# Optimization experiments

Hardware: AMD Instinct MI355X
Metric: run time of the kernel (lower is better)

Reference implementation:

```python
import jax, jax.numpy as jnp
import numpy as np

N_NODES = 100000
N_EDGES = 3200000
N_RELS = 8
F_IN = 64
F_OUT = 64


def setup_inputs() -> dict:
    key = jax.random.key(0)
    k1, k2, k3, k4, k5, k6 = jax.random.split(key, 6)
    X = jax.random.normal(k1, (N_NODES, F_IN), dtype=jnp.float32)
    W = jax.random.normal(k2, (N_RELS, F_IN, F_OUT), dtype=jnp.float32) * 0.1
    A = jax.random.uniform(k3, (N_EDGES,), dtype=jnp.float32)
    src = jax.random.randint(k4, (N_EDGES,), 0, N_NODES, dtype=jnp.int32)
    dst = jax.random.randint(k5, (N_EDGES,), 0, N_NODES, dtype=jnp.int32)
    etype = jax.random.randint(k6, (N_EDGES,), 0, N_RELS, dtype=jnp.int32)
    return {"X": X, "W": W, "A": A, "src": src, "dst": dst, "etype": etype}


def reference(X, W, A, src, dst, etype):
    # RGCN hetero forward: Y[i,fo] = sum_{r,j in N_r(i)} A[r,i,j] * (X[j] @ W[r])[fo]
    # Precompute per-relation transformed features: [R, N, F_out]
    XW = jnp.einsum('nf,rfo->rno', X, W)
    # Gather per-edge message and scale by edge weight: [E, F_out]
    msg = XW[etype, src] * A[:, None]
    # Scatter-add into destination nodes: [N, F_out]
    Y = jax.ops.segment_sum(msg, dst, num_segments=X.shape[0])
    return Y
```

## Files before the change

kernel.cpp:

```cpp
#include <hip/hip_runtime.h>
#include <hip/hip_fp16.h>

#define FDIM 64
#define SB 200
#define P_BLK 1024
#define NB_MAX 400
#define BKT_NODES 256
#define CHUNK_CAP 3200

typedef __attribute__((ext_vector_type(8))) short short8;
typedef __attribute__((ext_vector_type(4))) float float4_;

__device__ __forceinline__ unsigned short f2bf(float x) {
    unsigned u = __float_as_uint(x);
    return (unsigned short)((u + 0x7FFF + ((u >> 16) & 1)) >> 16);
}

__global__ __launch_bounds__(256) void xw_gemm_mfma(
    const float* __restrict__ X, const float* __restrict__ Wmat,
    __half* __restrict__ XWh, int N, int R)
{
    __shared__ unsigned short Wt[4 * 64 * 72];
    const int tid  = threadIdx.x;
    const int lane = tid & 63;
    const int wave = tid >> 6;
    const int quad = lane >> 4;
    const int l15  = lane & 15;
    const int blockBase = blockIdx.x * 256;

    short8 bfrag[4][2];
    bool tvalid[4];
#pragma unroll
    for (int t = 0; t < 4; ++t) {
        const int tb = blockBase + (wave * 4 + t) * 16;
        tvalid[t] = (tb < N);
        if (tvalid[t]) {
            const float* xp = X + (size_t)(tb + l15) * FDIM + quad * 8;
            const float4 x0 = *(const float4*)(xp);
            const float4 x1 = *(const float4*)(xp + 4);
            const float4 x2 = *(const float4*)(xp + 32);
            const float4 x3 = *(const float4*)(xp + 36);
            short8 b0, b1;
            b0[0]=f2bf(x0.x); b0[1]=f2bf(x0.y); b0[2]=f2bf(x0.z); b0[3]=f2bf(x0.w);
            b0[4]=f2bf(x1.x); b0[5]=f2bf(x1.y); b0[6]=f2bf(x1.z); b0[7]=f2bf(x1.w);
            b1[0]=f2bf(x2.x); b1[1]=f2bf(x2.y); b1[2]=f2bf(x2.z); b1[3]=f2bf(x2.w);
            b1[4]=f2bf(x3.x); b1[5]=f2bf(x3.y); b1[6]=f2bf(x3.z); b1[7]=f2bf(x3.w);
            bfrag[t][0] = b0; bfrag[t][1] = b1;
        } else {
            bfrag[t][0] = (short8)(0); bfrag[t][1] = (short8)(0);
        }
    }

    for (int rp = 0; rp < 2; ++rp) {
        __syncthreads();
#pragma unroll
        for (int it = 0; it < 16; ++it) {
            const int idx = it * 256 + tid;
            const int k  = idx & 63;
            const int f4 = (idx >> 6) & 15;
            const int r  = idx >> 10;
            const float4 w = *(const float4*)(Wmat + (((size_t)(rp * 4 + r) * FDIM + k) * FDIM + f4 * 4));
            const int base = (r * 64 + f4 * 4) * 72 + k;
            Wt[base + 0 * 72] = f2bf(w.x);
            Wt[base + 1 * 72] = f2bf(w.y);
            Wt[base + 2 * 72] = f2bf(w.z);
            Wt[base + 3 * 72] = f2bf(w.w);
        }
        __syncthreads();

#pragma unroll
        for (int t = 0; t < 4; ++t) {
            if (!tvalid[t]) continue;
            const int tb = blockBase + (wave * 4 + t) * 16;
            const int node = tb + l15;
#pragma unroll
            for (int r = 0; r < 4; ++r) {
                __half* orow = XWh + ((size_t)(rp * 4 + r) * N + node) * FDIM;
#pragma unroll
                for (int ft = 0; ft < 4; ++ft) {
                    const int f = ft * 16 + l15;
                    const unsigned short* wp = &Wt[(r * 64 + f) * 72 + quad * 8];
                    const short8 a0 = *(const short8*)(wp);
                    const short8 a1 = *(const short8*)(wp + 32);
                    float4_ acc = {0.f, 0.f, 0.f, 0.f};
                    acc = __builtin_amdgcn_mfma_f32_16x16x32_bf16(a0, bfrag[t][0], acc, 0, 0, 0);
                    acc = __builtin_amdgcn_mfma_f32_16x16x32_bf16(a1, bfrag[t][1], acc, 0, 0, 0);
                    const __half2 h01 = __floats2half2_rn(acc[0], acc[1]);
                    const __half2 h23 = __floats2half2_rn(acc[2], acc[3]);
                    uint2 st;
                    st.x = *(const unsigned*)&h01;
                    st.y = *(const unsigned*)&h23;
                    *(uint2*)(orow + ft * 16 + quad * 4) = st;
                }
            }
        }
    }
}

__global__ __launch_bounds__(256) void bin_hist(
    const int* __restrict__ dst, int* __restrict__ cnt, int E, int B, int chunk)
{
    __shared__ int lh[NB_MAX];
    const int p = blockIdx.x, tid = threadIdx.x;
    for (int b = tid; b < B; b += 256) lh[b] = 0;
    __syncthreads();
    const int i0 = p * chunk, iend = min(i0 + chunk, E);
    for (int i = i0 + tid; i < iend; i += 256)
        atomicAdd(&lh[dst[i] >> 8], 1);
    __syncthreads();
    for (int b = tid; b < B; b += 256) cnt[(size_t)b * P_BLK + p] = lh[b];
}

__global__ __launch_bounds__(256) void scan_partial(
    const int* __restrict__ cnt, int* __restrict__ blockSums, int M, int CH)
{
    __shared__ int sh[256];
    const int b = blockIdx.x, tid = threadIdx.x;
    const int i0 = b * CH, iend = min(i0 + CH, M);
    int s = 0;
    for (int i = i0 + tid; i < iend; i += 256) s += cnt[i];
    sh[tid] = s; __syncthreads();
    for (int off = 128; off > 0; off >>= 1) {
        if (tid < off) sh[tid] += sh[tid + off];
        __syncthreads();
    }
    if (tid == 0) blockSums[b] = sh[0];
}

__global__ __launch_bounds__(256) void scan_block(int* blockSums, int nb)
{
    __shared__ int sh[256];
    const int tid = threadIdx.x;
    const int v = (tid < nb) ? blockSums[tid] : 0;
    sh[tid] = v; __syncthreads();
    for (int off = 1; off < 256; off <<= 1) {
        const int t = (tid >= off) ? sh[tid - off] : 0;
        __syncthreads();
        sh[tid] += t;
        __syncthreads();
    }
    if (tid < nb) blockSums[tid] = sh[tid] - v;
}

__global__ __launch_bounds__(64) void scan_final(
    const int* __restrict__ cnt, const int* __restrict__ blockSums,
    int* __restrict__ offs, int M, int CH, int E)
{
    const int b = blockIdx.x, lane = threadIdx.x;
    const int i0 = b * CH, iend = min(i0 + CH, M);
    int carry = blockSums[b];
    for (int t = i0; t < iend; t += 64) {
        const int i = t + lane;
        const int c = (i < iend) ? cnt[i] : 0;
        int v = c;
#pragma unroll
        for (int o = 1; o < 64; o <<= 1) {
            const int u = __shfl_up(v, o, 64);
            if (lane >= o) v += u;
        }
        if (i < iend) offs[i] = carry + v - c;
        carry += __shfl(v, 63, 64);
    }
    if (b == (int)gridDim.x - 1 && lane == 0) offs[M] = E;
}

__global__ __launch_bounds__(256) void bin_scatter(
    const int* __restrict__ src, const int* __restrict__ dst,
    const int* __restrict__ etype, const float* __restrict__ A,
    const int* __restrict__ offs, int2* __restrict__ packed,
    int E, int N, int B, int chunk)
{
    __shared__ int lcnt[NB_MAX];
    __shared__ int lpfx[NB_MAX];
    __shared__ int gb[NB_MAX];
    __shared__ int2 recs[CHUNK_CAP];
    __shared__ unsigned short rbkt[CHUNK_CAP];
    const int p = blockIdx.x, tid = threadIdx.x;
    const int i0 = p * chunk, iend = min(i0 + chunk, E);

    for (int b = tid; b < B; b += 256) lcnt[b] = 0;
    __syncthreads();
    for (int i = i0 + tid; i < iend; i += 256)
        atomicAdd(&lcnt[dst[i] >> 8], 1);
    __syncthreads();

    if (tid < 64) {
        int carry = 0;
        for (int t0 = 0; t0 < B; t0 += 64) {
            const int b = t0 + tid;
            const int c = (b < B) ? lcnt[b] : 0;
            int v = c;
#pragma unroll
            for (int o = 1; o < 64; o <<= 1) {
                const int u = __shfl_up(v, o, 64);
                if (tid >= o) v += u;
            }
            if (b < B) lpfx[b] = carry + v - c;
            carry += __shfl(v, 63, 64);
        }
    }
    __syncthreads();
    for (int b = tid; b < B; b += 256) {
        gb[b] = offs[(size_t)b * P_BLK + p] - lpfx[b];
        lcnt[b] = lpfx[b];
    }
    __syncthreads();

    for (int i = i0 + tid; i < iend; i += 256) {
        const int d = dst[i];
        const int b = d >> 8;
        const int slot = atomicAdd(&lcnt[b], 1);
        recs[slot] = make_int2((etype[i] * N + src[i]) | ((d & 255) << 20),
                               __float_as_int(A[i]));
        rbkt[slot] = (unsigned short)b;
    }
    __syncthreads();

    const int tot = iend - i0;
    for (int s = tid; s < tot; s += 256)
        packed[gb[rbkt[s]] + s] = recs[s];
}

__global__ __launch_bounds__(1024) void bucket_sort(
    const int2* __restrict__ packed, const int* __restrict__ offs,
    int2* __restrict__ sorted, int* __restrict__ nodeOffs, int N, int B, int E)
{
    __shared__ int hist[BKT_NODES];
    __shared__ int pfx[BKT_NODES + 1];
    __shared__ int cur[BKT_NODES];
    const int bkt = blockIdx.x, tid = threadIdx.x;
    const int beg = offs[(size_t)bkt * P_BLK];
    const int end = (bkt + 1 < B) ? offs[(size_t)(bkt + 1) * P_BLK] : E;

    if (tid < BKT_NODES) hist[tid] = 0;
    __syncthreads();
    for (int i = beg + tid; i < end; i += 1024)
        atomicAdd(&hist[(packed[i].x >> 20) & (BKT_NODES - 1)], 1);
    __syncthreads();
    if (tid == 0) {
        int s = 0;
        pfx[0] = 0;
        for (int i = 0; i < BKT_NODES; ++i) { s += hist[i]; pfx[i + 1] = s; }
    }
    __syncthreads();
    if (tid < BKT_NODES) {
        cur[tid] = pfx[tid];
        const int n = bkt * BKT_NODES + tid;
        if (n < N) nodeOffs[n] = beg + pfx[tid];
    }
    if (bkt == B - 1 && tid == 0) nodeOffs[N] = E;
    __syncthreads();
    for (int i = beg + tid; i < end; i += 1024) {
        const int2 rec = packed[i];
        const int dl = (rec.x >> 20) & (BKT_NODES - 1);
        const int pos = atomicAdd(&cur[dl], 1);
        sorted[beg + pos] = rec;
    }
}

__global__ __launch_bounds__(256) void dst_aggregate(
    const __half* __restrict__ XWh, const int* __restrict__ nodeOffs,
    const int2* __restrict__ sorted, float* __restrict__ Y, int N)
{
    const int lane = threadIdx.x & 63;
    const int el   = lane >> 4;
    const int fl4  = lane & 15;
    const int wave = (int)((blockIdx.x * blockDim.x + threadIdx.x) >> 6);
    const int nWaves = (int)((gridDim.x * blockDim.x) >> 6);
    const __half2* __restrict__ XW2 = (const __half2*)XWh;
    const unsigned foff = (unsigned)(fl4 << 1);

    int d = wave;
    if (d >= N) return;
    int beg = nodeOffs[d];
    int end = nodeOffs[d + 1];

    while (d < N) {
        const int dn = d + nWaves;
        int nbeg = 0, nend = 0;
        if (dn < N) { nbeg = nodeOffs[dn]; nend = nodeOffs[dn + 1]; }

        float4_ acc = {0.f, 0.f, 0.f, 0.f};
        for (int base = beg; base < end; base += 64) {
            const int idx = base + lane;
            const int2 ka = (idx < end) ? sorted[idx] : make_int2(0, 0);
            const int nb = min(64, end - base);
            const int nsteps = (((nb + 3) >> 2) + 7) & ~7;
            for (int s = 0; s < nsteps; s += 8) {
                int k[8], b[8];
#pragma unroll
                for (int u = 0; u < 8; ++u) {
                    const int j = ((s + u) << 2) + el;
                    k[u] = __shfl(ka.x, j, 64);
                    b[u] = __shfl(ka.y, j, 64);
                }
                uint2 v[8];
#pragma unroll
                for (int u = 0; u < 8; ++u)
                    v[u] = *(const uint2*)(XW2 + ((((unsigned)k[u]) & 0xFFFFFu) << 5) + foff);
#pragma unroll
                for (int u = 0; u < 8; ++u) {
                    const float a = __int_as_float(b[u]);
                    const float2 f0 = __half22float2(*(const __half2*)&v[u].x);
                    const float2 f1 = __half22float2(*(const __half2*)&v[u].y);
                    acc[0] += a * f0.x; acc[1] += a * f0.y;
                    acc[2] += a * f1.x; acc[3] += a * f1.y;
                }
            }
        }
#pragma unroll
        for (int m = 16; m <= 32; m <<= 1) {
            acc[0] += __shfl_xor(acc[0], m, 64);
            acc[1] += __shfl_xor(acc[1], m, 64);
            acc[2] += __shfl_xor(acc[2], m, 64);
            acc[3] += __shfl_xor(acc[3], m, 64);
        }
        if (lane < 16)
            *(float4_*)(Y + (size_t)d * FDIM + (fl4 << 2)) = acc;

        d = dn; beg = nbeg; end = nend;
    }
}

extern "C" void kernel_launch(void* const* d_in, const int* in_sizes, int n_in,
                              void* d_out, int out_size, void* d_ws, size_t ws_size,
                              hipStream_t stream)
{
    const float* X     = (const float*)d_in[0];
    const float* Wmat  = (const float*)d_in[1];
    const float* A     = (const float*)d_in[2];
    const int*   src   = (const int*)d_in[3];
    const int*   dst   = (const int*)d_in[4];
    const int*   etype = (const int*)d_in[5];
    float* Y = (float*)d_out;

    const int N = in_sizes[0] / FDIM;
    const int R = in_sizes[1] / (FDIM * FDIM);
    const int E = in_sizes[2];
    (void)n_in; (void)out_size; (void)ws_size;

    const int B = (N + BKT_NODES - 1) / BKT_NODES;
    const int M = B * P_BLK;
    const int chunk = (E + P_BLK - 1) / P_BLK;
    const int CH = (M + SB - 1) / SB;

    char* ws = (char*)d_ws;
    size_t off = 0;
    auto take = [&](size_t bytes) { char* p = ws + off; off = (off + bytes + 255) & ~(size_t)255; return p; };
    __half* XWh      = (__half*)take((size_t)R * N * FDIM * sizeof(__half));
    int2*   packed   = (int2*)  take((size_t)E * sizeof(int2));
    int2*   sorted   = (int2*)  take((size_t)E * sizeof(int2));
    int*    cnt      = (int*)   take((size_t)M * sizeof(int));
    int*    offs     = (int*)   take((size_t)(M + 1) * sizeof(int));
    int*    nodeOffs = (int*)   take((size_t)(N + 1) * sizeof(int));
    int*    bsums    = (int*)   take((size_t)SB * sizeof(int));

    xw_gemm_mfma<<<(N + 255) / 256, 256, 0, stream>>>(X, Wmat, XWh, N, R);

    bin_hist<<<P_BLK, 256, 0, stream>>>(dst, cnt, E, B, chunk);
    scan_partial<<<SB, 256, 0, stream>>>(cnt, bsums, M, CH);
    scan_block<<<1, 256, 0, stream>>>(bsums, SB);
    scan_final<<<SB, 64, 0, stream>>>(cnt, bsums, offs, M, CH, E);
    bin_scatter<<<P_BLK, 256, 0, stream>>>(src, dst, etype, A, offs, packed, E, N, B, chunk);
    bucket_sort<<<B, 1024, 0, stream>>>(packed, offs, sorted, nodeOffs, N, B, E);

    dst_aggregate<<<2048, 256, 0, stream>>>(XWh, nodeOffs, sorted, Y, N);
}
```

Before: 312.4 us.

## Replace per-block histogram scan with global bucket atomics; stage GEMM output via LDS

```diff
diff --git a/kernel.cpp b/kernel.cpp
--- a/kernel.cpp
+++ b/kernel.cpp
@@ -2,7 +2,6 @@
 #include <hip/hip_fp16.h>
 
 #define FDIM 64
-#define SB 200
 #define P_BLK 1024
 #define NB_MAX 400
 #define BKT_NODES 256
@@ -21,6 +20,7 @@
     __half* __restrict__ XWh, int N, int R)
 {
     __shared__ unsigned short Wt[4 * 64 * 72];
+    __shared__ unsigned short Ot[4][16 * 72];
     const int tid  = threadIdx.x;
     const int lane = tid & 63;
     const int wave = tid >> 6;
@@ -72,10 +72,8 @@
         for (int t = 0; t < 4; ++t) {
             if (!tvalid[t]) continue;
             const int tb = blockBase + (wave * 4 + t) * 16;
-            const int node = tb + l15;
 #pragma unroll
             for (int r = 0; r < 4; ++r) {
-                __half* orow = XWh + ((size_t)(rp * 4 + r) * N + node) * FDIM;
 #pragma unroll
                 for (int ft = 0; ft < 4; ++ft) {
                     const int f = ft * 16 + l15;
@@ -90,84 +88,63 @@
                     uint2 st;
                     st.x = *(const unsigned*)&h01;
                     st.y = *(const unsigned*)&h23;
-                    *(uint2*)(orow + ft * 16 + quad * 4) = st;
+                    *(uint2*)&Ot[wave][l15 * 72 + ft * 16 + quad * 4] = st;
                 }
+                const int node = lane >> 2;
+                const int c    = lane & 3;
+                const uint4 w0 = *(const uint4*)&Ot[wave][node * 72 + c * 16];
+                const uint4 w1 = *(const uint4*)&Ot[wave][node * 72 + c * 16 + 8];
+                __half* orow = XWh + ((size_t)(rp * 4 + r) * N + (tb + node)) * FDIM;
+                *(uint4*)(orow + c * 16)     = w0;
+                *(uint4*)(orow + c * 16 + 8) = w1;
             }
         }
     }
 }
 
-__global__ __launch_bounds__(256) void bin_hist(
-    const int* __restrict__ dst, int* __restrict__ cnt, int E, int B, int chunk)
+__global__ __launch_bounds__(256) void bucket_count(
+    const int* __restrict__ dst, int* __restrict__ bcnt, int E, int B)
 {
     __shared__ int lh[NB_MAX];
-    const int p = blockIdx.x, tid = threadIdx.x;
+    const int tid = threadIdx.x;
     for (int b = tid; b < B; b += 256) lh[b] = 0;
     __syncthreads();
-    const int i0 = p * chunk, iend = min(i0 + chunk, E);
-    for (int i = i0 + tid; i < iend; i += 256)
+    const int stride = (int)gridDim.x * 256;
+    for (int i = (int)blockIdx.x * 256 + tid; i < E; i += stride)
         atomicAdd(&lh[dst[i] >> 8], 1);
     __syncthreads();
-    for (int b = tid; b < B; b += 256) cnt[(size_t)b * P_BLK + p] = lh[b];
-}
-
-__global__ __launch_bounds__(256) void scan_partial(
-    const int* __restrict__ cnt, int* __restrict__ blockSums, int M, int CH)
-{
-    __shared__ int sh[256];
-    const int b = blockIdx.x, tid = threadIdx.x;
-    const int i0 = b * CH, iend = min(i0 + CH, M);
-    int s = 0;
-    for (int i = i0 + tid; i < iend; i += 256) s += cnt[i];
-    sh[tid] = s; __syncthreads();
-    for (int off = 128; off > 0; off >>= 1) {
-        if (tid < off) sh[tid] += sh[tid + off];
-        __syncthreads();
-    }
-    if (tid == 0) blockSums[b] = sh[0];
-}
-
-__global__ __launch_bounds__(256) void scan_block(int* blockSums, int nb)
-{
-    __shared__ int sh[256];
+    for (int b = tid; b < B; b += 256) {
+        const int c = lh[b];
+        if (c) atomicAdd(&bcnt[b], c);
+    }
+}
+
+__global__ __launch_bounds__(512) void bucket_scan(
+    const int* __restrict__ bcnt, int* __restrict__ base,
+    int* __restrict__ gcur, int B, int E)
+{
+    __shared__ int sh[512];
     const int tid = threadIdx.x;
-    const int v = (tid < nb) ? blockSums[tid] : 0;
+    const int v = (tid < B) ? bcnt[tid] : 0;
     sh[tid] = v; __syncthreads();
-    for (int off = 1; off < 256; off <<= 1) {
+    for (int off = 1; off < 512; off <<= 1) {
         const int t = (tid >= off) ? sh[tid - off] : 0;
         __syncthreads();
         sh[tid] += t;
         __syncthreads();
     }
-    if (tid < nb) blockSums[tid] = sh[tid] - v;
-}
-
-__global__ __launch_bounds__(64) void scan_final(
-    const int* __restrict__ cnt, const int* __restrict__ blockSums,
-    int* __restrict__ offs, int M, int CH, int E)
-{
-    const int b = blockIdx.x, lane = threadIdx.x;
-    const int i0 = b * CH, iend = min(i0 + CH, M);
-    int carry = blockSums[b];
-    for (int t = i0; t < iend; t += 64) {
-        const int i = t + lane;
-        const int c = (i < iend) ? cnt[i] : 0;
-        int v = c;
-#pragma unroll
-        for (int o = 1; o < 64; o <<= 1) {
-            const int u = __shfl_up(v, o, 64);
-            if (lane >= o) v += u;
-        }
-        if (i < iend) offs[i] = carry + v - c;
-        carry += __shfl(v, 63, 64);
-    }
-    if (b == (int)gridDim.x - 1 && lane == 0) offs[M] = E;
+    if (tid < B) {
+        const int e = sh[tid] - v;
+        base[tid] = e;
+        gcur[tid] = e;
+    }
+    if (tid == 0) base[B] = E;
 }
 
 __global__ __launch_bounds__(256) void bin_scatter(
     const int* __restrict__ src, const int* __restrict__ dst,
     const int* __restrict__ etype, const float* __restrict__ A,
-    const int* __restrict__ offs, int2* __restrict__ packed,
+    int* __restrict__ gcur, int2* __restrict__ packed,
     int E, int N, int B, int chunk)
 {
     __shared__ int lcnt[NB_MAX];
@@ -201,7 +178,9 @@
     }
     __syncthreads();
     for (int b = tid; b < B; b += 256) {
-        gb[b] = offs[(size_t)b * P_BLK + p] - lpfx[b];
+        const int c = lcnt[b];
+        const int rbase = c ? atomicAdd(&gcur[b], c) : 0;
+        gb[b] = rbase - lpfx[b];
         lcnt[b] = lpfx[b];
     }
     __syncthreads();
@@ -222,15 +201,15 @@
 }
 
 __global__ __launch_bounds__(1024) void bucket_sort(
-    const int2* __restrict__ packed, const int* __restrict__ offs,
+    const int2* __restrict__ packed, const int* __restrict__ base,
     int2* __restrict__ sorted, int* __restrict__ nodeOffs, int N, int B, int E)
 {
     __shared__ int hist[BKT_NODES];
     __shared__ int pfx[BKT_NODES + 1];
     __shared__ int cur[BKT_NODES];
     const int bkt = blockIdx.x, tid = threadIdx.x;
-    const int beg = offs[(size_t)bkt * P_BLK];
-    const int end = (bkt + 1 < B) ? offs[(size_t)(bkt + 1) * P_BLK] : E;
+    const int beg = base[bkt];
+    const int end = base[bkt + 1];
 
     if (tid < BKT_NODES) hist[tid] = 0;
     __syncthreads();
@@ -281,10 +260,10 @@
         if (dn < N) { nbeg = nodeOffs[dn]; nend = nodeOffs[dn + 1]; }
 
         float4_ acc = {0.f, 0.f, 0.f, 0.f};
-        for (int base = beg; base < end; base += 64) {
-            const int idx = base + lane;
+        for (int base2 = beg; base2 < end; base2 += 64) {
+            const int idx = base2 + lane;
             const int2 ka = (idx < end) ? sorted[idx] : make_int2(0, 0);
-            const int nb = min(64, end - base);
+            const int nb = min(64, end - base2);
             const int nsteps = (((nb + 3) >> 2) + 7) & ~7;
             for (int s = 0; s < nsteps; s += 8) {
                 int k[8], b[8];
@@ -340,9 +319,7 @@
     (void)n_in; (void)out_size; (void)ws_size;
 
     const int B = (N + BKT_NODES - 1) / BKT_NODES;
-    const int M = B * P_BLK;
     const int chunk = (E + P_BLK - 1) / P_BLK;
-    const int CH = (M + SB - 1) / SB;
 
     char* ws = (char*)d_ws;
     size_t off = 0;
@@ -350,19 +327,19 @@
     __half* XWh      = (__half*)take((size_t)R * N * FDIM * sizeof(__half));
     int2*   packed   = (int2*)  take((size_t)E * sizeof(int2));
     int2*   sorted   = (int2*)  take((size_t)E * sizeof(int2));
-    int*    cnt      = (int*)   take((size_t)M * sizeof(int));
-    int*    offs     = (int*)   take((size_t)(M + 1) * sizeof(int));
+    int*    bcnt     = (int*)   take((size_t)B * sizeof(int));
+    int*    base     = (int*)   take((size_t)(B + 1) * sizeof(int));
+    int*    gcur     = (int*)   take((size_t)B * sizeof(int));
     int*    nodeOffs = (int*)   take((size_t)(N + 1) * sizeof(int));
-    int*    bsums    = (int*)   take((size_t)SB * sizeof(int));
+
+    hipMemsetAsync(bcnt, 0, (size_t)B * sizeof(int), stream);
 
     xw_gemm_mfma<<<(N + 255) / 256, 256, 0, stream>>>(X, Wmat, XWh, N, R);
 
-    bin_hist<<<P_BLK, 256, 0, stream>>>(dst, cnt, E, B, chunk);
-    scan_partial<<<SB, 256, 0, stream>>>(cnt, bsums, M, CH);
-    scan_block<<<1, 256, 0, stream>>>(bsums, SB);
-    scan_final<<<SB, 64, 0, stream>>>(cnt, bsums, offs, M, CH, E);
-    bin_scatter<<<P_BLK, 256, 0, stream>>>(src, dst, etype, A, offs, packed, E, N, B, chunk);
-    bucket_sort<<<B, 1024, 0, stream>>>(packed, offs, sorted, nodeOffs, N, B, E);
+    bucket_count<<<512, 256, 0, stream>>>(dst, bcnt, E, B);
+    bucket_scan<<<1, 512, 0, stream>>>(bcnt, base, gcur, B, E);
+    bin_scatter<<<P_BLK, 256, 0, stream>>>(src, dst, etype, A, gcur, packed, E, N, B, chunk);
+    bucket_sort<<<B, 1024, 0, stream>>>(packed, base, sorted, nodeOffs, N, B, E);
 
     dst_aggregate<<<2048, 256, 0, stream>>>(XWh, nodeOffs, sorted, Y, N);
 }
```

Result: no change. 317.2 us (+1.5%).
